# Kernel optimization log

Hardware: AMD Instinct MI355X
Metric: run time of the kernel (lower is better)

Reference implementation:

```python
import jax, jax.numpy as jnp
import numpy as np

B, S, D, H = 2, 2048, 1024, 16
Dh = D // H

def setup_inputs() -> dict:
    key = jax.random.key(0)
    ks = jax.random.split(key, 11)
    def lin(k, fan_in):
        bound = 1.0 / np.sqrt(fan_in)
        kw, kb = jax.random.split(k)
        W = jax.random.uniform(kw, (D, D), jnp.float32, -bound, bound)
        b = jax.random.uniform(kb, (D,), jnp.float32, -bound, bound)
        return W, b
    Wq, bq = lin(ks[0], D)
    Wk, bk = lin(ks[1], D)
    Wv, bv = lin(ks[2], D)
    Wo, bo = lin(ks[3], D)
    Q = jax.random.normal(ks[4], (B, S, D), jnp.float32)
    K = jax.random.normal(ks[5], (B, S, D), jnp.float32)
    V = jax.random.normal(ks[6], (B, S, D), jnp.float32)
    return {"Q": Q, "K": K, "V": V, "Wq": Wq, "bq": bq, "Wk": Wk, "bk": bk,
            "Wv": Wv, "bv": bv, "Wo": Wo, "bo": bo}

def _split_heads(x):
    # [B,S,D] -> [B,H,S,Dh]
    b, s, _ = x.shape
    return x.reshape(b, s, H, Dh).transpose(0, 2, 1, 3)

def reference(Q, K, V, Wq, bq, Wk, bk, Wv, bv, Wo, bo):
    q = _split_heads(Q @ Wq.T + bq)
    k = _split_heads(K @ Wk.T + bk)
    v = _split_heads(V @ Wv.T + bv)
    scores = jnp.einsum('bhqd,bhkd->bhqk', q, k) / jnp.sqrt(jnp.float32(Dh))
    attn = jax.nn.softmax(scores, axis=-1)
    out = jnp.einsum('bhqk,bhkd->bhqd', attn, v)  # [B,H,S,Dh]
    out = out.transpose(0, 2, 1, 3).reshape(Q.shape[0], Q.shape[1], D)
    return out @ Wo.T + bo
```

## Files before the change

kernel.cpp:

```cpp
#include <hip/hip_runtime.h>

#define SEQ 2048
#define DMODEL 1024
#define NH 16
#define DH 64

typedef __attribute__((ext_vector_type(8))) short bf16x8;
typedef __attribute__((ext_vector_type(4))) short bf16x4;
typedef __attribute__((ext_vector_type(4))) float floatx4;
typedef __attribute__((ext_vector_type(4))) unsigned short u16x4;
typedef unsigned short u16;
typedef unsigned int u32;

typedef const void __attribute__((address_space(1)))* as1cvp;
typedef void __attribute__((address_space(3)))* as3vp;

__device__ __forceinline__ void glds16(const void* g, void* l) {
    __builtin_amdgcn_global_load_lds((as1cvp)g, (as3vp)l, 16, 0, 0);
}

__device__ __forceinline__ u16 f2bf(float f) {
    union { u32 u; float f; } v; v.f = f;
    return (u16)((v.u + 0x8000u) >> 16);
}

__device__ __forceinline__ u32 pk2(float a, float b) {
    union { u32 u; float f; } x, y; x.f = a; y.f = b;
    u32 xr = x.u + 0x8000u, yr = y.u + 0x8000u;
#if __has_builtin(__builtin_amdgcn_perm)
    return __builtin_amdgcn_perm(yr, xr, 0x07060302u);
#else
    return (xr >> 16) | (yr & 0xffff0000u);
#endif
}

__device__ __forceinline__ float ex2(float x) {
#if __has_builtin(__builtin_amdgcn_exp2f)
    return __builtin_amdgcn_exp2f(x);
#else
    float r; asm("v_exp_f32 %0, %1" : "=v"(r) : "v"(x)); return r;
#endif
}

__device__ __forceinline__ floatx4 mfma16(bf16x4 a, bf16x4 b, floatx4 c) {
#if __has_builtin(__builtin_amdgcn_mfma_f32_16x16x16bf16_1k)
    return __builtin_amdgcn_mfma_f32_16x16x16bf16_1k(a, b, c, 0, 0, 0);
#else
    asm volatile("v_mfma_f32_16x16x16_bf16 %0, %1, %2, %0" : "+v"(c) : "v"(a), "v"(b));
    return c;
#endif
}

__device__ __forceinline__ uint4 cvt8(const float* __restrict__ p) {
    float4 a = *(const float4*)p;
    float4 b = *(const float4*)(p + 4);
    uint4 q;
    q.x = pk2(a.x, a.y); q.y = pk2(a.z, a.w);
    q.z = pk2(b.x, b.y); q.w = pk2(b.z, b.w);
    return q;
}

#define QSCALE 0.18033688011112042f

__global__ __launch_bounds__(256) void cvt_all(
    const float* __restrict__ Q, const float* __restrict__ K, const float* __restrict__ V,
    const float* __restrict__ W0, const float* __restrict__ W1,
    const float* __restrict__ W2, const float* __restrict__ W3,
    u16* __restrict__ Qb, u16* __restrict__ Kb, u16* __restrict__ Vb,
    u16* __restrict__ Wb)
{
    const int y = blockIdx.y;
    const float* src; u16* dst;
    if (y == 0)      { src = Q;  dst = Qb; }
    else if (y == 1) { src = K;  dst = Kb; }
    else if (y == 2) { src = V;  dst = Vb; }
    else {
        if (blockIdx.x >= 512) return;
        src = (y == 3) ? W0 : (y == 4) ? W1 : (y == 5) ? W2 : W3;
        dst = Wb + (size_t)(y - 3) * 1048576;
    }
    size_t i = ((size_t)blockIdx.x * 256 + threadIdx.x) * 8;
    *(uint4*)(dst + i) = cvt8(src + i);
}

__global__ __launch_bounds__(256) void cvt_w(
    const float* __restrict__ W0, const float* __restrict__ W1,
    const float* __restrict__ W2, const float* __restrict__ W3,
    u16* __restrict__ out)
{
    const float* src = (blockIdx.y == 0) ? W0 : (blockIdx.y == 1) ? W1
                     : (blockIdx.y == 2) ? W2 : W3;
    size_t i = ((size_t)blockIdx.x * 256 + threadIdx.x) * 8;
    *(uint4*)(out + (size_t)blockIdx.y * 1048576 + i) = cvt8(src + i);
}

__device__ __forceinline__ void qkv_store(
    int z, u16* __restrict__ outp, int rowg, int col, floatx4 a4, float bv, float sc)
{
    union { u32 w[2]; u16 h[4]; u16x4 v4; } pk;
    pk.w[0] = pk2((a4[0] + bv) * sc, (a4[1] + bv) * sc);
    pk.w[1] = pk2((a4[2] + bv) * sc, (a4[3] + bv) * sc);
    int b = rowg >> 11, s = rowg & 2047, h = col >> 6, d = col & 63;
    if (z < 2) {
#pragma unroll
        for (int r = 0; r < 4; r++)
            outp[((size_t)(b * NH + h) * SEQ + s + r) * DH + d] = pk.h[r];
    } else {
        *(u16x4*)(outp + ((size_t)(b * NH + h) * DH + d) * SEQ + s) = pk.v4;
    }
}

__global__ __launch_bounds__(256) void gemm_qkv_bb(
    const u16* __restrict__ Qb, const u16* __restrict__ Kb, const u16* __restrict__ Vb,
    const u16* __restrict__ Wb,
    const float* __restrict__ b0, const float* __restrict__ b1, const float* __restrict__ b2,
    u16* __restrict__ qo, u16* __restrict__ ko, u16* __restrict__ vto)
{
    __shared__ __align__(16) u16 As[128 * 32];
    __shared__ __align__(16) u16 Bs[128 * 32];
    const int tid = threadIdx.x, l = tid & 63, w = tid >> 6;
    const int lm = l & 15, quad = l >> 4;
    const int wr = (w >> 1) * 64, wc = (w & 1) * 64;
    const int bm = blockIdx.y * 128, bn = blockIdx.x * 128;
    const int z = blockIdx.z;
    const u16* A      = (z == 0) ? Qb : (z == 1) ? Kb : Vb;
    const u16* W      = Wb + (size_t)z * 1048576;
    const float* bias = (z == 0) ? b0 : (z == 1) ? b1 : b2;

    const int srow = tid >> 2, scol = (tid & 3) * 8;

    floatx4 acc[4][4];
#pragma unroll
    for (int i = 0; i < 4; i++)
#pragma unroll
        for (int j = 0; j < 4; j++) acc[i][j] = (floatx4){0.f, 0.f, 0.f, 0.f};

    for (int kt = 0; kt < DMODEL; kt += 32) {
        __syncthreads();
        glds16(A + (size_t)(bm + srow) * DMODEL + kt + scol, As + w * 512);
        glds16(A + (size_t)(bm + 64 + srow) * DMODEL + kt + scol, As + 2048 + w * 512);
        glds16(W + (size_t)(bn + srow) * DMODEL + kt + scol, Bs + w * 512);
        glds16(W + (size_t)(bn + 64 + srow) * DMODEL + kt + scol, Bs + 2048 + w * 512);
        __syncthreads();

        bf16x8 af[4], bfr[4];
#pragma unroll
        for (int mi = 0; mi < 4; mi++)
            af[mi] = *(const bf16x8*)(As + (wr + mi * 16 + lm) * 32 + quad * 8);
#pragma unroll
        for (int ni = 0; ni < 4; ni++)
            bfr[ni] = *(const bf16x8*)(Bs + (wc + ni * 16 + lm) * 32 + quad * 8);
#pragma unroll
        for (int mi = 0; mi < 4; mi++)
#pragma unroll
            for (int ni = 0; ni < 4; ni++)
                acc[mi][ni] = __builtin_amdgcn_mfma_f32_16x16x32_bf16(
                    af[mi], bfr[ni], acc[mi][ni], 0, 0, 0);
    }

    const float sc = (z == 0) ? QSCALE : 1.0f;
    u16* outp = (z == 0) ? qo : (z == 1) ? ko : vto;
#pragma unroll
    for (int ni = 0; ni < 4; ni++) {
        int col = bn + wc + ni * 16 + lm;
        float bv = bias[col];
#pragma unroll
        for (int mi = 0; mi < 4; mi++)
            qkv_store(z, outp, bm + wr + mi * 16 + quad * 4, col, acc[mi][ni], bv, sc);
    }
}

template<bool WBF>
__global__ __launch_bounds__(256) void gemm_qkv(
    const float* __restrict__ Qf, const float* __restrict__ Kf, const float* __restrict__ Vf,
    const void* __restrict__ W0, const void* __restrict__ W1, const void* __restrict__ W2,
    const float* __restrict__ b0, const float* __restrict__ b1, const float* __restrict__ b2,
    u16* __restrict__ qo, u16* __restrict__ ko, u16* __restrict__ vto)
{
    __shared__ __align__(16) u16 As[128 * 32];
    __shared__ __align__(16) u16 Bs[128 * 32];
    const int tid = threadIdx.x, l = tid & 63, w = tid >> 6;
    const int lm = l & 15, quad = l >> 4;
    const int wr = (w >> 1) * 64, wc = (w & 1) * 64;
    const int bm = blockIdx.y * 128, bn = blockIdx.x * 128;
    const int z = blockIdx.z;
    const float* A    = (z == 0) ? Qf : (z == 1) ? Kf : Vf;
    const void* Wp    = (z == 0) ? W0 : (z == 1) ? W1 : W2;
    const float* bias = (z == 0) ? b0 : (z == 1) ? b1 : b2;

    floatx4 acc[4][4];
#pragma unroll
    for (int i = 0; i < 4; i++)
#pragma unroll
        for (int j = 0; j < 4; j++) acc[i][j] = (floatx4){0.f, 0.f, 0.f, 0.f};

    for (int kt = 0; kt < DMODEL; kt += 32) {
        __syncthreads();
#pragma unroll
        for (int j = 0; j < 2; j++) {
            int ch = j * 256 + tid, row = ch >> 2, c = ch & 3;
            *(uint4*)(As + ch * 8) = cvt8(A + (size_t)(bm + row) * DMODEL + kt + c * 8);
        }
        if (WBF) {
            const u16* Wb = (const u16*)Wp;
            glds16(Wb + (size_t)(bn + (tid >> 2)) * DMODEL + kt + (tid & 3) * 8, Bs + w * 512);
            glds16(Wb + (size_t)(bn + 64 + (tid >> 2)) * DMODEL + kt + (tid & 3) * 8, Bs + 2048 + w * 512);
        } else {
            const float* Wf = (const float*)Wp;
#pragma unroll
            for (int j = 0; j < 2; j++) {
                int ch = j * 256 + tid, row = ch >> 2, c = ch & 3;
                *(uint4*)(Bs + ch * 8) = cvt8(Wf + (size_t)(bn + row) * DMODEL + kt + c * 8);
            }
        }
        __syncthreads();

        bf16x8 af[4], bfr[4];
#pragma unroll
        for (int mi = 0; mi < 4; mi++)
            af[mi] = *(const bf16x8*)(As + (wr + mi * 16 + lm) * 32 + quad * 8);
#pragma unroll
        for (int ni = 0; ni < 4; ni++)
            bfr[ni] = *(const bf16x8*)(Bs + (wc + ni * 16 + lm) * 32 + quad * 8);
#pragma unroll
        for (int mi = 0; mi < 4; mi++)
#pragma unroll
            for (int ni = 0; ni < 4; ni++)
                acc[mi][ni] = __builtin_amdgcn_mfma_f32_16x16x32_bf16(
                    af[mi], bfr[ni], acc[mi][ni], 0, 0, 0);
    }

    const float sc = (z == 0) ? QSCALE : 1.0f;
    u16* outp = (z == 0) ? qo : (z == 1) ? ko : vto;
#pragma unroll
    for (int ni = 0; ni < 4; ni++) {
        int col = bn + wc + ni * 16 + lm;
        float bv = bias[col];
#pragma unroll
        for (int mi = 0; mi < 4; mi++)
            qkv_store(z, outp, bm + wr + mi * 16 + quad * 4, col, acc[mi][ni], bv, sc);
    }
}

template<bool WBF>
__global__ __launch_bounds__(256) void gemm_o(
    const u16* __restrict__ A, const void* __restrict__ Wp,
    const float* __restrict__ bias, float* __restrict__ out)
{
    __shared__ __align__(16) u16 As[128 * 32];
    __shared__ __align__(16) u16 Bs[64 * 32];
    const int tid = threadIdx.x, l = tid & 63, w = tid >> 6;
    const int lm = l & 15, quad = l >> 4;
    const int bm = blockIdx.y * 128, bn = blockIdx.x * 64;

    floatx4 acc[2][4];
#pragma unroll
    for (int i = 0; i < 2; i++)
#pragma unroll
        for (int j = 0; j < 4; j++) acc[i][j] = (floatx4){0.f, 0.f, 0.f, 0.f};

    for (int kt = 0; kt < DMODEL; kt += 32) {
        __syncthreads();
        glds16(A + (size_t)(bm + (tid >> 2)) * DMODEL + kt + (tid & 3) * 8, As + w * 512);
        glds16(A + (size_t)(bm + 64 + (tid >> 2)) * DMODEL + kt + (tid & 3) * 8, As + 2048 + w * 512);
        if (WBF) {
            glds16((const u16*)Wp + (size_t)(bn + (tid >> 2)) * DMODEL + kt + (tid & 3) * 8, Bs + w * 512);
        } else {
            *(uint4*)(Bs + tid * 8) =
                cvt8((const float*)Wp + (size_t)(bn + (tid >> 2)) * DMODEL + kt + (tid & 3) * 8);
        }
        __syncthreads();

        bf16x8 af[2], bfr[4];
#pragma unroll
        for (int mi = 0; mi < 2; mi++)
            af[mi] = *(const bf16x8*)(As + (w * 32 + mi * 16 + lm) * 32 + quad * 8);
#pragma unroll
        for (int ni = 0; ni < 4; ni++)
            bfr[ni] = *(const bf16x8*)(Bs + (ni * 16 + lm) * 32 + quad * 8);
#pragma unroll
        for (int mi = 0; mi < 2; mi++)
#pragma unroll
            for (int ni = 0; ni < 4; ni++)
                acc[mi][ni] = __builtin_amdgcn_mfma_f32_16x16x32_bf16(
                    af[mi], bfr[ni], acc[mi][ni], 0, 0, 0);
    }

#pragma unroll
    for (int ni = 0; ni < 4; ni++) {
        int col = bn + ni * 16 + lm;
        float bv = bias[col];
#pragma unroll
        for (int mi = 0; mi < 2; mi++) {
#pragma unroll
            for (int r = 0; r < 4; r++) {
                int rowg = bm + w * 32 + mi * 16 + quad * 4 + r;
                out[(size_t)rowg * DMODEL + col] = acc[mi][ni][r] + bv;
            }
        }
    }
}

#define SP 72
#define TS (64 * SP)
#define BUFSZ (4 * TS)
__global__ __launch_bounds__(512, 4) void attn_kernel(
    const u16* __restrict__ q, const u16* __restrict__ k,
    const u16* __restrict__ vt, u16* __restrict__ out)
{
    __shared__ __align__(16) u16 smem[2 * BUFSZ];
    const int tid = threadIdx.x, l = tid & 63, w = tid >> 6;
    const int lm = l & 15, quad = l >> 4;
    const int qt = blockIdx.x, bh = blockIdx.y;
    const int b = bh >> 4, h = bh & 15;
    const int rg = w & 3, half = w >> 2;

    bf16x8 qf[2][2];
#pragma unroll
    for (int nt = 0; nt < 2; nt++) {
        int row = qt * 128 + rg * 32 + nt * 16 + lm;
        const u16* qp = q + ((size_t)bh * SEQ + row) * DH;
        qf[nt][0] = *(const bf16x8*)(qp + quad * 8);
        qf[nt][1] = *(const bf16x8*)(qp + 32 + quad * 8);
    }

    floatx4 O[4][2];
#pragma unroll
    for (int dt = 0; dt < 4; dt++)
#pragma unroll
        for (int nt = 0; nt < 2; nt++) O[dt][nt] = (floatx4){0.f, 0.f, 0.f, 0.f};
    floatx4 Ol[2] = {(floatx4){0.f,0.f,0.f,0.f}, (floatx4){0.f,0.f,0.f,0.f}};

    const bf16x4 onesb = {(short)0x3F80, (short)0x3F80, (short)0x3F80, (short)0x3F80};

    const int srow = tid >> 3, scol = (tid & 7) * 8;
    const int pb0 = ((scol >> 2) & 3) * 16 + (scol >> 4) * 4;
    const u16* kbase = k + (size_t)bh * SEQ * DH;
    const u16* vbase = vt + (size_t)bh * DH * SEQ;

    uint4 krA, krB, vrA, vrB;
#define LOADT(T) do { \
        const u16* kg = kbase + (size_t)(T) * 64 * DH; \
        const u16* vg = vbase + (size_t)(T) * 64; \
        krA = *(const uint4*)(kg + (size_t)srow * DH + scol); \
        krB = *(const uint4*)(kg + (size_t)(1024 + srow) * DH + scol); \
        vrA = *(const uint4*)(vg + (size_t)srow * SEQ + scol); \
        vrB = *(const uint4*)(vg + (size_t)srow * SEQ + 1024 + scol); \
    } while (0)
#define WRBUF(BUF) do { \
        u16* K0 = smem + (BUF) * BUFSZ; \
        u16* K1 = K0 + TS; \
        u16* V0 = K0 + 2 * TS; \
        u16* V1 = K0 + 3 * TS; \
        *(uint4*)(K0 + srow * SP + scol) = krA; \
        *(uint4*)(K1 + srow * SP + scol) = krB; \
        *(uint2*)(V0 + srow * SP + pb0)      = make_uint2(vrA.x, vrA.y); \
        *(uint2*)(V0 + srow * SP + pb0 + 16) = make_uint2(vrA.z, vrA.w); \
        *(uint2*)(V1 + srow * SP + pb0)      = make_uint2(vrB.x, vrB.y); \
        *(uint2*)(V1 + srow * SP + pb0 + 16) = make_uint2(vrB.z, vrB.w); \
    } while (0)

    LOADT(0);
    WRBUF(0);
    LOADT(1);
    __syncthreads();

    for (int t = 0; t < 16; t++) {
        const int cur = t & 1;
        const u16* Kh = smem + cur * BUFSZ + half * TS;
        const u16* Vh = smem + cur * BUFSZ + (2 + half) * TS;

        floatx4 Sc[4][2];
        __builtin_amdgcn_s_setprio(1);
#pragma unroll
        for (int mt = 0; mt < 4; mt++) {
            bf16x8 ka0 = *(const bf16x8*)(Kh + (mt * 16 + lm) * SP + quad * 8);
            bf16x8 ka1 = *(const bf16x8*)(Kh + (mt * 16 + lm) * SP + 32 + quad * 8);
#pragma unroll
            for (int nt = 0; nt < 2; nt++) {
                floatx4 c = (floatx4){0.f, 0.f, 0.f, 0.f};
                c = __builtin_amdgcn_mfma_f32_16x16x32_bf16(ka0, qf[nt][0], c, 0, 0, 0);
                c = __builtin_amdgcn_mfma_f32_16x16x32_bf16(ka1, qf[nt][1], c, 0, 0, 0);
                Sc[mt][nt] = c;
            }
        }
        __builtin_amdgcn_s_setprio(0);

        bf16x4 pb[4][2];
#pragma unroll
        for (int nt = 0; nt < 2; nt++) {
#pragma unroll
            for (int mt = 0; mt < 4; mt++) {
#pragma unroll
                for (int r = 0; r < 4; r++) Sc[mt][nt][r] = ex2(Sc[mt][nt][r]);
                union { u32 w2[2]; bf16x4 v; } pku;
                pku.w2[0] = pk2(Sc[mt][nt][0], Sc[mt][nt][1]);
                pku.w2[1] = pk2(Sc[mt][nt][2], Sc[mt][nt][3]);
                pb[mt][nt] = pku.v;
            }
        }

        __builtin_amdgcn_s_setprio(1);
#pragma unroll
        for (int nt = 0; nt < 2; nt++) {
            Ol[nt] = mfma16(onesb, pb[0][nt], Ol[nt]);
            Ol[nt] = mfma16(onesb, pb[1][nt], Ol[nt]);
            Ol[nt] = mfma16(onesb, pb[2][nt], Ol[nt]);
            Ol[nt] = mfma16(onesb, pb[3][nt], Ol[nt]);
        }

#pragma unroll
        for (int dt = 0; dt < 4; dt++) {
            const u16* vp = Vh + (dt * 16 + lm) * SP + quad * 16;
            bf16x8 v8a = *(const bf16x8*)vp;
            bf16x8 v8b = *(const bf16x8*)(vp + 8);
            bf16x4 va0 = __builtin_shufflevector(v8a, v8a, 0, 1, 2, 3);
            bf16x4 va1 = __builtin_shufflevector(v8a, v8a, 4, 5, 6, 7);
            bf16x4 va2 = __builtin_shufflevector(v8b, v8b, 0, 1, 2, 3);
            bf16x4 va3 = __builtin_shufflevector(v8b, v8b, 4, 5, 6, 7);
            O[dt][0] = mfma16(va0, pb[0][0], O[dt][0]);
            O[dt][1] = mfma16(va0, pb[0][1], O[dt][1]);
            O[dt][0] = mfma16(va1, pb[1][0], O[dt][0]);
            O[dt][1] = mfma16(va1, pb[1][1], O[dt][1]);
            O[dt][0] = mfma16(va2, pb[2][0], O[dt][0]);
            O[dt][1] = mfma16(va2, pb[2][1], O[dt][1]);
            O[dt][0] = mfma16(va3, pb[3][0], O[dt][0]);
            O[dt][1] = mfma16(va3, pb[3][1], O[dt][1]);
        }
        __builtin_amdgcn_s_setprio(0);

        if (t + 1 < 16) {
            WRBUF(cur ^ 1);
            if (t + 2 < 16) LOADT(t + 2);
        }
        __syncthreads();
    }
#undef LOADT
#undef WRBUF

    float* obuf  = (float*)smem;
    float* mlbuf = (float*)smem + 8192;
    if (w >= 4) {
#pragma unroll
        for (int nt = 0; nt < 2; nt++) {
            float* ob = obuf + (((rg * 64 + l) * 2 + nt) << 4);
#pragma unroll
            for (int dt = 0; dt < 4; dt++)
                *(floatx4*)(ob + dt * 4) = O[dt][nt];
            mlbuf[(rg * 64 + l) * 2 + nt] = Ol[nt][0];
        }
    }
    __syncthreads();
    if (w < 4) {
#pragma unroll
        for (int nt = 0; nt < 2; nt++) {
            float* ob = obuf + (((rg * 64 + l) * 2 + nt) << 4);
            float lB = mlbuf[(rg * 64 + l) * 2 + nt];
            float inv = 1.0f / (Ol[nt][0] + lB);
            int s = qt * 128 + rg * 32 + nt * 16 + lm;
            u16* op = out + ((size_t)b * SEQ + s) * DMODEL + h * DH;
#pragma unroll
            for (int dt = 0; dt < 4; dt++) {
                floatx4 Ob = *(const floatx4*)(ob + dt * 4);
                union { u32 w2[2]; u16x4 v; } pku;
                pku.w2[0] = pk2((O[dt][nt][0] + Ob[0]) * inv,
                                (O[dt][nt][1] + Ob[1]) * inv);
                pku.w2[1] = pk2((O[dt][nt][2] + Ob[2]) * inv,
                                (O[dt][nt][3] + Ob[3]) * inv);
                *(u16x4*)(op + dt * 16 + quad * 4) = pku.v;
            }
        }
    }
}

extern "C" void kernel_launch(void* const* d_in, const int* in_sizes, int n_in,
                              void* d_out, int out_size, void* d_ws, size_t ws_size,
                              hipStream_t stream) {
    (void)in_sizes; (void)n_in; (void)out_size;
    const float* Q  = (const float*)d_in[0];
    const float* K  = (const float*)d_in[1];
    const float* V  = (const float*)d_in[2];
    const float* Wq = (const float*)d_in[3];
    const float* bq = (const float*)d_in[4];
    const float* Wk = (const float*)d_in[5];
    const float* bk = (const float*)d_in[6];
    const float* Wv = (const float*)d_in[7];
    const float* bv = (const float*)d_in[8];
    const float* Wo = (const float*)d_in[9];
    const float* bo = (const float*)d_in[10];

    const size_t NEL = (size_t)2 * NH * SEQ * DH;
    u16* base = (u16*)d_ws;
    dim3 bb(256);
    dim3 ab(512);

    if (ws_size >= 8 * NEL * 2) {
        u16* Qb   = base;
        u16* Kb   = Qb + NEL;
        u16* Vb   = Kb + NEL;
        u16* Wb   = Vb + NEL;
        u16* qws  = Wb + NEL;
        u16* kws  = qws + NEL;
        u16* vtws = kws + NEL;
        u16* aws  = vtws + NEL;
        cvt_all<<<dim3(2048, 7), bb, 0, stream>>>(Q, K, V, Wq, Wk, Wv, Wo, Qb, Kb, Vb, Wb);
        gemm_qkv_bb<<<dim3(8, 32, 3), bb, 0, stream>>>(
            Qb, Kb, Vb, Wb, bq, bk, bv, qws, kws, vtws);
        attn_kernel<<<dim3(SEQ / 128, 2 * NH), ab, 0, stream>>>(qws, kws, vtws, aws);
        gemm_o<true><<<dim3(16, 32), bb, 0, stream>>>(aws, Wb + 3145728, bo, (float*)d_out);
    } else if (ws_size >= 5 * NEL * 2) {
        u16* Wb = base;
        u16* qws = base + NEL; u16* kws = qws + NEL; u16* vtws = kws + NEL; u16* aws = vtws + NEL;
        cvt_w<<<dim3(512, 4), bb, 0, stream>>>(Wq, Wk, Wv, Wo, Wb);
        gemm_qkv<true><<<dim3(8, 32, 3), bb, 0, stream>>>(
            Q, K, V, Wb, Wb + 1048576, Wb + 2097152, bq, bk, bv, qws, kws, vtws);
        attn_kernel<<<dim3(SEQ / 128, 2 * NH), ab, 0, stream>>>(qws, kws, vtws, aws);
        gemm_o<true><<<dim3(16, 32), bb, 0, stream>>>(aws, Wb + 3145728, bo, (float*)d_out);
    } else {
        u16* qws = base; u16* kws = qws + NEL; u16* vtws = kws + NEL; u16* aws = vtws + NEL;
        gemm_qkv<false><<<dim3(8, 32, 3), bb, 0, stream>>>(
            Q, K, V, Wq, Wk, Wv, bq, bk, bv, qws, kws, vtws);
        attn_kernel<<<dim3(SEQ / 128, 2 * NH), ab, 0, stream>>>(qws, kws, vtws, aws);
        gemm_o<false><<<dim3(16, 32), bb, 0, stream>>>(aws, Wo, bo, (float*)d_out);
    }
}
```

Before: 234.6 us.

## Triple-buffer QKV and output GEMMs and software-pipeline the attention loop

Both projection GEMMs now use a three-stage LDS ring filled by global_load_lds. Loads for tile i+2 are issued while tile i is computed, and vmcnt waits with a raw barrier replace the two syncthreads per iteration. The attention loop is software-pipelined so that QK^T and exp for tile t overlap the PV product for tile t-1, using two alternating P register sets. The intent is to hide global and LDS latency behind MFMA work, at the cost of more LDS, more registers and tighter manual waitcnt/barrier correctness.

Measured after the change: 279.4 us. 19.1% more time.

```diff
diff --git a/kernel.cpp b/kernel.cpp
--- a/kernel.cpp
+++ b/kernel.cpp
@@ -116,8 +116,8 @@
     const float* __restrict__ b0, const float* __restrict__ b1, const float* __restrict__ b2,
     u16* __restrict__ qo, u16* __restrict__ ko, u16* __restrict__ vto)
 {
-    __shared__ __align__(16) u16 As[128 * 32];
-    __shared__ __align__(16) u16 Bs[128 * 32];
+    __shared__ __align__(16) u16 As[3][4096];
+    __shared__ __align__(16) u16 Bs[3][4096];
     const int tid = threadIdx.x, l = tid & 63, w = tid >> 6;
     const int lm = l & 15, quad = l >> 4;
     const int wr = (w >> 1) * 64, wc = (w & 1) * 64;
@@ -135,28 +135,47 @@
 #pragma unroll
         for (int j = 0; j < 4; j++) acc[i][j] = (floatx4){0.f, 0.f, 0.f, 0.f};
 
-    for (int kt = 0; kt < DMODEL; kt += 32) {
-        __syncthreads();
-        glds16(A + (size_t)(bm + srow) * DMODEL + kt + scol, As + w * 512);
-        glds16(A + (size_t)(bm + 64 + srow) * DMODEL + kt + scol, As + 2048 + w * 512);
-        glds16(W + (size_t)(bn + srow) * DMODEL + kt + scol, Bs + w * 512);
-        glds16(W + (size_t)(bn + 64 + srow) * DMODEL + kt + scol, Bs + 2048 + w * 512);
-        __syncthreads();
-
+#define QKV_STAGE(I, NB) do { \
+        const int kt_ = (I) * 32; \
+        glds16(A + (size_t)(bm + srow) * DMODEL + kt_ + scol, As[NB] + w * 512); \
+        glds16(A + (size_t)(bm + 64 + srow) * DMODEL + kt_ + scol, As[NB] + 2048 + w * 512); \
+        glds16(W + (size_t)(bn + srow) * DMODEL + kt_ + scol, Bs[NB] + w * 512); \
+        glds16(W + (size_t)(bn + 64 + srow) * DMODEL + kt_ + scol, Bs[NB] + 2048 + w * 512); \
+    } while (0)
+
+    QKV_STAGE(0, 0);
+    QKV_STAGE(1, 1);
+    asm volatile("s_waitcnt vmcnt(4)" ::: "memory");
+    __builtin_amdgcn_s_barrier();
+
+    int cur = 0, nx = 2;
+    for (int i = 0; i < 32; i++) {
         bf16x8 af[4], bfr[4];
 #pragma unroll
         for (int mi = 0; mi < 4; mi++)
-            af[mi] = *(const bf16x8*)(As + (wr + mi * 16 + lm) * 32 + quad * 8);
+            af[mi] = *(const bf16x8*)(As[cur] + (wr + mi * 16 + lm) * 32 + quad * 8);
 #pragma unroll
         for (int ni = 0; ni < 4; ni++)
-            bfr[ni] = *(const bf16x8*)(Bs + (wc + ni * 16 + lm) * 32 + quad * 8);
+            bfr[ni] = *(const bf16x8*)(Bs[cur] + (wc + ni * 16 + lm) * 32 + quad * 8);
 #pragma unroll
         for (int mi = 0; mi < 4; mi++)
 #pragma unroll
             for (int ni = 0; ni < 4; ni++)
                 acc[mi][ni] = __builtin_amdgcn_mfma_f32_16x16x32_bf16(
                     af[mi], bfr[ni], acc[mi][ni], 0, 0, 0);
-    }
+
+        if (i + 2 < 32) {
+            QKV_STAGE(i + 2, nx);
+            asm volatile("s_waitcnt vmcnt(4)" ::: "memory");
+            __builtin_amdgcn_s_barrier();
+        } else if (i + 1 < 32) {
+            asm volatile("s_waitcnt vmcnt(0)" ::: "memory");
+            __builtin_amdgcn_s_barrier();
+        }
+        cur = (cur == 2) ? 0 : cur + 1;
+        nx  = (nx == 2) ? 0 : nx + 1;
+    }
+#undef QKV_STAGE
 
     const float sc = (z == 0) ? QSCALE : 1.0f;
     u16* outp = (z == 0) ? qo : (z == 1) ? ko : vto;
@@ -242,6 +261,78 @@
     }
 }
 
+__global__ __launch_bounds__(256) void gemm_o_p(
+    const u16* __restrict__ A, const u16* __restrict__ W,
+    const float* __restrict__ bias, float* __restrict__ out)
+{
+    __shared__ __align__(16) u16 As[3][4096];
+    __shared__ __align__(16) u16 Bs[3][2048];
+    const int tid = threadIdx.x, l = tid & 63, w = tid >> 6;
+    const int lm = l & 15, quad = l >> 4;
+    const int bm = blockIdx.y * 128, bn = blockIdx.x * 64;
+
+    floatx4 acc[2][4];
+#pragma unroll
+    for (int i = 0; i < 2; i++)
+#pragma unroll
+        for (int j = 0; j < 4; j++) acc[i][j] = (floatx4){0.f, 0.f, 0.f, 0.f};
+
+#define O_STAGE(I, NB) do { \
+        const int kt_ = (I) * 32; \
+        glds16(A + (size_t)(bm + (tid >> 2)) * DMODEL + kt_ + (tid & 3) * 8, As[NB] + w * 512); \
+        glds16(A + (size_t)(bm + 64 + (tid >> 2)) * DMODEL + kt_ + (tid & 3) * 8, As[NB] + 2048 + w * 512); \
+        glds16(W + (size_t)(bn + (tid >> 2)) * DMODEL + kt_ + (tid & 3) * 8, Bs[NB] + w * 512); \
+    } while (0)
+
+    O_STAGE(0, 0);
+    O_STAGE(1, 1);
+    asm volatile("s_waitcnt vmcnt(3)" ::: "memory");
+    __builtin_amdgcn_s_barrier();
+
+    int cur = 0, nx = 2;
+    for (int i = 0; i < 32; i++) {
+        bf16x8 af[2], bfr[4];
+#pragma unroll
+        for (int mi = 0; mi < 2; mi++)
+            af[mi] = *(const bf16x8*)(As[cur] + (w * 32 + mi * 16 + lm) * 32 + quad * 8);
+#pragma unroll
+        for (int ni = 0; ni < 4; ni++)
+            bfr[ni] = *(const bf16x8*)(Bs[cur] + (ni * 16 + lm) * 32 + quad * 8);
+#pragma unroll
+        for (int mi = 0; mi < 2; mi++)
+#pragma unroll
+            for (int ni = 0; ni < 4; ni++)
+                acc[mi][ni] = __builtin_amdgcn_mfma_f32_16x16x32_bf16(
+                    af[mi], bfr[ni], acc[mi][ni], 0, 0, 0);
+
+        if (i + 2 < 32) {
+            O_STAGE(i + 2, nx);
+            asm volatile("s_waitcnt vmcnt(3)" ::: "memory");
+            __builtin_amdgcn_s_barrier();
+        } else if (i + 1 < 32) {
+            asm volatile("s_waitcnt vmcnt(0)" ::: "memory");
+            __builtin_amdgcn_s_barrier();
+        }
+        cur = (cur == 2) ? 0 : cur + 1;
+        nx  = (nx == 2) ? 0 : nx + 1;
+    }
+#undef O_STAGE
+
+#pragma unroll
+    for (int ni = 0; ni < 4; ni++) {
+        int col = bn + ni * 16 + lm;
+        float bv = bias[col];
+#pragma unroll
+        for (int mi = 0; mi < 2; mi++) {
+#pragma unroll
+            for (int r = 0; r < 4; r++) {
+                int rowg = bm + w * 32 + mi * 16 + quad * 4 + r;
+                out[(size_t)rowg * DMODEL + col] = acc[mi][ni][r] + bv;
+            }
+        }
+    }
+}
+
 template<bool WBF>
 __global__ __launch_bounds__(256) void gemm_o(
     const u16* __restrict__ A, const void* __restrict__ Wp,
@@ -304,6 +395,58 @@
 #define SP 72
 #define TS (64 * SP)
 #define BUFSZ (4 * TS)
+
+__device__ __forceinline__ void qk_exp_step(
+    const u16* Kh, const bf16x8 (&qf)[2][2], int lm, int quad, bf16x4 (&pb)[4][2])
+{
+#pragma unroll
+    for (int mt = 0; mt < 4; mt++) {
+        bf16x8 ka0 = *(const bf16x8*)(Kh + (mt * 16 + lm) * SP + quad * 8);
+        bf16x8 ka1 = *(const bf16x8*)(Kh + (mt * 16 + lm) * SP + 32 + quad * 8);
+#pragma unroll
+        for (int nt = 0; nt < 2; nt++) {
+            floatx4 c = (floatx4){0.f, 0.f, 0.f, 0.f};
+            c = __builtin_amdgcn_mfma_f32_16x16x32_bf16(ka0, qf[nt][0], c, 0, 0, 0);
+            c = __builtin_amdgcn_mfma_f32_16x16x32_bf16(ka1, qf[nt][1], c, 0, 0, 0);
+            union { u32 w2[2]; bf16x4 v; } pku;
+            pku.w2[0] = pk2(ex2(c[0]), ex2(c[1]));
+            pku.w2[1] = pk2(ex2(c[2]), ex2(c[3]));
+            pb[mt][nt] = pku.v;
+        }
+    }
+}
+
+__device__ __forceinline__ void pv_step(
+    const u16* Vh, const bf16x4 (&pb)[4][2], int lm, int quad,
+    floatx4 (&O)[4][2], floatx4 (&Ol)[2], bf16x4 onesb)
+{
+#pragma unroll
+    for (int nt = 0; nt < 2; nt++) {
+        Ol[nt] = mfma16(onesb, pb[0][nt], Ol[nt]);
+        Ol[nt] = mfma16(onesb, pb[1][nt], Ol[nt]);
+        Ol[nt] = mfma16(onesb, pb[2][nt], Ol[nt]);
+        Ol[nt] = mfma16(onesb, pb[3][nt], Ol[nt]);
+    }
+#pragma unroll
+    for (int dt = 0; dt < 4; dt++) {
+        const u16* vp = Vh + (dt * 16 + lm) * SP + quad * 16;
+        bf16x8 v8a = *(const bf16x8*)vp;
+        bf16x8 v8b = *(const bf16x8*)(vp + 8);
+        bf16x4 va0 = __builtin_shufflevector(v8a, v8a, 0, 1, 2, 3);
+        bf16x4 va1 = __builtin_shufflevector(v8a, v8a, 4, 5, 6, 7);
+        bf16x4 va2 = __builtin_shufflevector(v8b, v8b, 0, 1, 2, 3);
+        bf16x4 va3 = __builtin_shufflevector(v8b, v8b, 4, 5, 6, 7);
+        O[dt][0] = mfma16(va0, pb[0][0], O[dt][0]);
+        O[dt][1] = mfma16(va0, pb[0][1], O[dt][1]);
+        O[dt][0] = mfma16(va1, pb[1][0], O[dt][0]);
+        O[dt][1] = mfma16(va1, pb[1][1], O[dt][1]);
+        O[dt][0] = mfma16(va2, pb[2][0], O[dt][0]);
+        O[dt][1] = mfma16(va2, pb[2][1], O[dt][1]);
+        O[dt][0] = mfma16(va3, pb[3][0], O[dt][0]);
+        O[dt][1] = mfma16(va3, pb[3][1], O[dt][1]);
+    }
+}
+
 __global__ __launch_bounds__(512, 4) void attn_kernel(
     const u16* __restrict__ q, const u16* __restrict__ k,
     const u16* __restrict__ vt, u16* __restrict__ out)
@@ -330,6 +473,7 @@
 #pragma unroll
         for (int nt = 0; nt < 2; nt++) O[dt][nt] = (floatx4){0.f, 0.f, 0.f, 0.f};
     floatx4 Ol[2] = {(floatx4){0.f,0.f,0.f,0.f}, (floatx4){0.f,0.f,0.f,0.f}};
+    bf16x4 pbA[4][2], pbB[4][2];
 
     const bf16x4 onesb = {(short)0x3F80, (short)0x3F80, (short)0x3F80, (short)0x3F80};
 
@@ -365,79 +509,42 @@
     LOADT(1);
     __syncthreads();
 
-    for (int t = 0; t < 16; t++) {
-        const int cur = t & 1;
-        const u16* Kh = smem + cur * BUFSZ + half * TS;
-        const u16* Vh = smem + cur * BUFSZ + (2 + half) * TS;
-
-        floatx4 Sc[4][2];
-        __builtin_amdgcn_s_setprio(1);
-#pragma unroll
-        for (int mt = 0; mt < 4; mt++) {
-            bf16x8 ka0 = *(const bf16x8*)(Kh + (mt * 16 + lm) * SP + quad * 8);
-            bf16x8 ka1 = *(const bf16x8*)(Kh + (mt * 16 + lm) * SP + 32 + quad * 8);
-#pragma unroll
-            for (int nt = 0; nt < 2; nt++) {
-                floatx4 c = (floatx4){0.f, 0.f, 0.f, 0.f};
-                c = __builtin_amdgcn_mfma_f32_16x16x32_bf16(ka0, qf[nt][0], c, 0, 0, 0);
-                c = __builtin_amdgcn_mfma_f32_16x16x32_bf16(ka1, qf[nt][1], c, 0, 0, 0);
-                Sc[mt][nt] = c;
-            }
-        }
-        __builtin_amdgcn_s_setprio(0);
-
-        bf16x4 pb[4][2];
-#pragma unroll
-        for (int nt = 0; nt < 2; nt++) {
-#pragma unroll
-            for (int mt = 0; mt < 4; mt++) {
-#pragma unroll
-                for (int r = 0; r < 4; r++) Sc[mt][nt][r] = ex2(Sc[mt][nt][r]);
-                union { u32 w2[2]; bf16x4 v; } pku;
-                pku.w2[0] = pk2(Sc[mt][nt][0], Sc[mt][nt][1]);
-                pku.w2[1] = pk2(Sc[mt][nt][2], Sc[mt][nt][3]);
-                pb[mt][nt] = pku.v;
-            }
-        }
-
-        __builtin_amdgcn_s_setprio(1);
-#pragma unroll
-        for (int nt = 0; nt < 2; nt++) {
-            Ol[nt] = mfma16(onesb, pb[0][nt], Ol[nt]);
-            Ol[nt] = mfma16(onesb, pb[1][nt], Ol[nt]);
-            Ol[nt] = mfma16(onesb, pb[2][nt], Ol[nt]);
-            Ol[nt] = mfma16(onesb, pb[3][nt], Ol[nt]);
-        }
-
-#pragma unroll
-        for (int dt = 0; dt < 4; dt++) {
-            const u16* vp = Vh + (dt * 16 + lm) * SP + quad * 16;
-            bf16x8 v8a = *(const bf16x8*)vp;
-            bf16x8 v8b = *(const bf16x8*)(vp + 8);
-            bf16x4 va0 = __builtin_shufflevector(v8a, v8a, 0, 1, 2, 3);
-            bf16x4 va1 = __builtin_shufflevector(v8a, v8a, 4, 5, 6, 7);
-            bf16x4 va2 = __builtin_shufflevector(v8b, v8b, 0, 1, 2, 3);
-            bf16x4 va3 = __builtin_shufflevector(v8b, v8b, 4, 5, 6, 7);
-            O[dt][0] = mfma16(va0, pb[0][0], O[dt][0]);
-            O[dt][1] = mfma16(va0, pb[0][1], O[dt][1]);
-            O[dt][0] = mfma16(va1, pb[1][0], O[dt][0]);
-            O[dt][1] = mfma16(va1, pb[1][1], O[dt][1]);
-            O[dt][0] = mfma16(va2, pb[2][0], O[dt][0]);
-            O[dt][1] = mfma16(va2, pb[2][1], O[dt][1]);
-            O[dt][0] = mfma16(va3, pb[3][0], O[dt][0]);
-            O[dt][1] = mfma16(va3, pb[3][1], O[dt][1]);
-        }
-        __builtin_amdgcn_s_setprio(0);
-
-        if (t + 1 < 16) {
-            WRBUF(cur ^ 1);
-            if (t + 2 < 16) LOADT(t + 2);
-        }
-        __syncthreads();
-    }
+    __builtin_amdgcn_s_setprio(1);
+    qk_exp_step(smem + half * TS, qf, lm, quad, pbA);
+    __builtin_amdgcn_s_setprio(0);
+    WRBUF(1);
+    LOADT(2);
+    asm volatile("s_waitcnt lgkmcnt(0)" ::: "memory");
+    __builtin_amdgcn_s_barrier();
+
+#define AITER(T, PBOLD, PBNEW) do { \
+        const u16* Kh_ = smem + ((T) & 1) * BUFSZ + half * TS; \
+        const u16* Vh_ = smem + (((T) - 1) & 1) * BUFSZ + (2 + half) * TS; \
+        __builtin_amdgcn_s_setprio(1); \
+        qk_exp_step(Kh_, qf, lm, quad, PBNEW); \
+        pv_step(Vh_, PBOLD, lm, quad, O, Ol, onesb); \
+        __builtin_amdgcn_s_setprio(0); \
+        __builtin_amdgcn_s_barrier(); \
+        WRBUF(((T) + 1) & 1); \
+        if ((T) + 2 < 16) LOADT((T) + 2); \
+        asm volatile("s_waitcnt lgkmcnt(0)" ::: "memory"); \
+        __builtin_amdgcn_s_barrier(); \
+    } while (0)
+
+    for (int td = 0; td < 7; td++) {
+        AITER(2 * td + 1, pbA, pbB);
+        AITER(2 * td + 2, pbB, pbA);
+    }
+    __builtin_amdgcn_s_setprio(1);
+    qk_exp_step(smem + BUFSZ + half * TS, qf, lm, quad, pbB);
+    pv_step(smem + (2 + half) * TS, pbA, lm, quad, O, Ol, onesb);
+    pv_step(smem + BUFSZ + (2 + half) * TS, pbB, lm, quad, O, Ol, onesb);
+    __builtin_amdgcn_s_setprio(0);
+#undef AITER
 #undef LOADT
 #undef WRBUF
 
+    __syncthreads();
     float* obuf  = (float*)smem;
     float* mlbuf = (float*)smem + 8192;
     if (w >= 4) {
@@ -507,7 +614,7 @@
         gemm_qkv_bb<<<dim3(8, 32, 3), bb, 0, stream>>>(
             Qb, Kb, Vb, Wb, bq, bk, bv, qws, kws, vtws);
         attn_kernel<<<dim3(SEQ / 128, 2 * NH), ab, 0, stream>>>(qws, kws, vtws, aws);
-        gemm_o<true><<<dim3(16, 32), bb, 0, stream>>>(aws, Wb + 3145728, bo, (float*)d_out);
+        gemm_o_p<<<dim3(16, 32), bb, 0, stream>>>(aws, Wb + 3145728, bo, (float*)d_out);
     } else if (ws_size >= 5 * NEL * 2) {
         u16* Wb = base;
         u16* qws = base + NEL; u16* kws = qws + NEL; u16* vtws = kws + NEL; u16* aws = vtws + NEL;
@@ -515,7 +622,7 @@
         gemm_qkv<true><<<dim3(8, 32, 3), bb, 0, stream>>>(
             Q, K, V, Wb, Wb + 1048576, Wb + 2097152, bq, bk, bv, qws, kws, vtws);
         attn_kernel<<<dim3(SEQ / 128, 2 * NH), ab, 0, stream>>>(qws, kws, vtws, aws);
-        gemm_o<true><<<dim3(16, 32), bb, 0, stream>>>(aws, Wb + 3145728, bo, (float*)d_out);
+        gemm_o_p<<<dim3(16, 32), bb, 0, stream>>>(aws, Wb + 3145728, bo, (float*)d_out);
     } else {
         u16* qws = base; u16* kws = qws + NEL; u16* vtws = kws + NEL; u16* aws = vtws + NEL;
         gemm_qkv<false><<<dim3(8, 32, 3), bb, 0, stream>>>(
```
